# Performance work log

Measured on AMD Instinct MI355X. Metric: run time of the kernel, lower is better.

## Reference

```python
import jax, jax.numpy as jnp
import numpy as np

DIM = 1024
N_HEADS = 16
HEAD_DIM = DIM // N_HEADS


def setup_inputs() -> dict:
    key = jax.random.key(0)
    ks = jax.random.split(key, 7)
    s = 1.0 / np.sqrt(DIM)
    return {
        "hidden_states": jax.random.normal(ks[0], (1, 4096, DIM), dtype=jnp.float32),
        "Wq": jax.random.uniform(ks[1], (DIM, DIM), jnp.float32, -s, s),
        "bq": jax.random.uniform(ks[2], (DIM,), jnp.float32, -s, s),
        "Wk": jax.random.uniform(ks[3], (DIM, DIM), jnp.float32, -s, s),
        "bk": jax.random.uniform(ks[4], (DIM,), jnp.float32, -s, s),
        "Wv": jax.random.uniform(ks[5], (DIM, DIM), jnp.float32, -s, s),
        "bv": jax.random.uniform(ks[6], (DIM,), jnp.float32, -s, s),
    }


def _split_heads(x):
    # [B, S, DIM] -> [B, H, S, HEAD_DIM]
    b, s, _ = x.shape
    return x.reshape(b, s, N_HEADS, HEAD_DIM).transpose(0, 2, 1, 3)


def reference(hidden_states, Wq, bq, Wk, bk, Wv, bv):
    q = _split_heads(hidden_states @ Wq + bq)
    k = _split_heads(hidden_states @ Wk + bk)
    v = _split_heads(hidden_states @ Wv + bv)
    scores = jnp.einsum("bhqd,bhkd->bhqk", q, k) / np.sqrt(HEAD_DIM).astype(np.float32)
    probs = jax.nn.softmax(scores, axis=-1)  # dropout prob = 0 -> identity
    ctx = jnp.einsum("bhqk,bhkd->bhqd", probs, v)
    b, h, s, d = ctx.shape
    return ctx.transpose(0, 2, 1, 3).reshape(b, s, h * d)
```

## Files before the change

kernel.cpp:

```cpp
#include <hip/hip_runtime.h>
#include <hip/hip_bf16.h>

#define S_LEN 4096
#define DIM   1024
#define NH    16
#define HD    64

typedef unsigned short u16;
typedef short  bf16x8 __attribute__((ext_vector_type(8)));
typedef float  f32x4  __attribute__((ext_vector_type(4)));

__device__ __forceinline__ u16 f2bf(float f){
  union { float f; unsigned u; } x; x.f = f;
  unsigned u = x.u;
  return (u16)((u + 0x7FFFu + ((u >> 16) & 1u)) >> 16);
}
__device__ __forceinline__ unsigned pk2(float a, float b){
  union { __hip_bfloat162 h; unsigned u; } x;
  x.h = __float22bfloat162_rn(float2{a, b});
  return x.u;
}
__device__ __forceinline__ void ld2lds16(const u16* g, u16* l){
  __builtin_amdgcn_global_load_lds((const __attribute__((address_space(1))) void*)g,
                                   (__attribute__((address_space(3))) void*)l, 16, 0, 0);
}

#define QSCALE 0.1803368801111204f

__global__ __launch_bounds__(256) void fill_sentinel(float* __restrict__ out, int n){
  int i = blockIdx.x * 256 + threadIdx.x;
  if (i < n) out[i] = 77.0f;
}

__global__ __launch_bounds__(256) void prep_fused(
    const float* __restrict__ X, u16* __restrict__ Xb,
    const float* __restrict__ W0, const float* __restrict__ W1, const float* __restrict__ W2,
    u16* __restrict__ Wt)
{
  __shared__ __align__(16) u16 tile[64*72];
  int b = blockIdx.x;
  int t = threadIdx.x;
  if (b < 2048){
    size_t i = ((size_t)b * 256 + t) * 8;
    float4 v0 = *(const float4*)(X + i);
    float4 v1 = *(const float4*)(X + i + 4);
    uint4 w;
    w.x = pk2(v0.x, v0.y); w.y = pk2(v0.z, v0.w);
    w.z = pk2(v1.x, v1.y); w.w = pk2(v1.z, v1.w);
    *(uint4*)(Xb + i) = w;
    return;
  }
  int tid = b - 2048;
  int z   = tid >> 8;
  int rem = tid & 255;
  int k0  = (rem & 15) * 64, n0 = (rem >> 4) * 64;
  const float* W = z==0 ? W0 : z==1 ? W1 : W2;
  u16* T = Wt + (size_t)z * DIM * DIM;
  #pragma unroll
  for (int i = 0; i < 4; ++i){
    int idx = t + i*256;
    int row = idx >> 4, col4 = (idx & 15) * 4;
    float4 v = *(const float4*)(W + (size_t)(k0+row)*DIM + n0 + col4);
    tile[(col4+0)*72 + row] = f2bf(v.x);
    tile[(col4+1)*72 + row] = f2bf(v.y);
    tile[(col4+2)*72 + row] = f2bf(v.z);
    tile[(col4+3)*72 + row] = f2bf(v.w);
  }
  __syncthreads();
  #pragma unroll
  for (int i = 0; i < 2; ++i){
    int idx = t + i*256;
    int n = idx >> 3, k16 = (idx & 7) * 8;
    *(int4*)(T + (size_t)(n0+n)*DIM + k0 + k16) = *(const int4*)(tile + n*72 + k16);
  }
}

__device__ __forceinline__ void qkv_epilogue(
    int z, int m0, int n0, int wm, int wn, int quad, int l15,
    const f32x4 acc[4][4], const float* bias,
    u16* __restrict__ qb, u16* __restrict__ kf_out, u16* __restrict__ vf_out)
{
  #pragma unroll
  for (int nt=0; nt<4; ++nt){
    int n = n0 + wn + nt*16 + l15;
    float bv = bias[n];
    int h = n >> 6, d = n & 63;
    #pragma unroll
    for (int mt=0; mt<4; ++mt){
      int mb = m0 + wm + mt*16 + quad*4;
      f32x4 c = acc[mt][nt];
      if (z == 0){
        #pragma unroll
        for (int r=0; r<4; ++r)
          qb[(size_t)(mb + r)*DIM + n] = f2bf((c[r] + bv) * QSCALE);
      } else if (z == 1){
        int half = d >> 5, quadk = (d >> 3) & 3, j = d & 7;
        #pragma unroll
        for (int r=0; r<4; ++r){
          int s = mb + r;
          size_t idx = ((((size_t)h*256 + (s >> 4))*2 + half)*64 + quadk*16 + (s & 15))*8 + j;
          kf_out[idx] = f2bf(c[r] + bv);
        }
      } else {
        int kt64 = mb >> 6;
        int kn   = (mb >> 4) & 3;
        int qsl  = (mb >> 2) & 3;
        int h2   = kn >> 1;
        int jj0  = (kn & 1) * 4;
        int dt = d >> 4, dl = d & 15;
        size_t base = (((((size_t)h*64 + kt64)*4 + dt)*2 + h2)*64 + qsl*16 + dl)*8 + jj0;
        ushort4 p;
        p.x = f2bf(c[0]+bv); p.y = f2bf(c[1]+bv);
        p.z = f2bf(c[2]+bv); p.w = f2bf(c[3]+bv);
        *(ushort4*)(vf_out + base) = p;
      }
    }
  }
}

__global__ __launch_bounds__(256) void qkv_gemm_fast(
    const u16* __restrict__ Xbf, const u16* __restrict__ Wt,
    const float* __restrict__ b0, const float* __restrict__ b1, const float* __restrict__ b2,
    u16* __restrict__ qb, u16* __restrict__ kf_out, u16* __restrict__ vf_out)
{
  int fid = blockIdx.x;
  int z   = fid >> 8;
  int r   = fid & 255;
  int m0  = (((r & 7) << 2) + ((r >> 3) & 3)) * 128;
  int n0  = (r >> 5) * 128;

  const u16* Wz = Wt + (size_t)z * DIM * DIM;
  const float* bias = z==0 ? b0 : z==1 ? b1 : b2;

  __shared__ __align__(16) u16 SMEM[128*136];
  u16* As = SMEM;
  u16* Bs = SMEM + 8192;

  int t = threadIdx.x, wave = t >> 6, lane = t & 63, quad = lane >> 4, l15 = lane & 15;
  int wm = (wave >> 1) * 64, wn = (wave & 1) * 64;

  f32x4 acc[4][4];
  #pragma unroll
  for (int i=0;i<4;++i)
    #pragma unroll
    for (int j=0;j<4;++j) acc[i][j] = (f32x4){0.f,0.f,0.f,0.f};

  int srow = wave*32 + (lane >> 2);
  int skc_g = (((lane & 3) ^ ((lane >> 3) & 3))) * 8;
  int skc_l = (lane & 3) * 8;
  const u16* gA0 = Xbf + (size_t)(m0 + srow)*DIM + skc_g;
  const u16* gA1 = gA0 + (size_t)16*DIM;
  const u16* gB0 = Wz  + (size_t)(n0 + srow)*DIM + skc_g;
  const u16* gB1 = gB0 + (size_t)16*DIM;
  u16* lA0 = As + srow*32 + skc_l;
  u16* lA1 = lA0 + 16*32;
  u16* lB0 = Bs + srow*32 + skc_l;
  u16* lB1 = lB0 + 16*32;

  int swz = (quad ^ ((l15 >> 1) & 3)) * 8;

#define GSTAGE(P, KO)                                                            \
  do {                                                                           \
    ld2lds16(gA0 + (KO), lA0 + (P)*4096);                                        \
    ld2lds16(gA1 + (KO), lA1 + (P)*4096);                                        \
    ld2lds16(gB0 + (KO), lB0 + (P)*4096);                                        \
    ld2lds16(gB1 + (KO), lB1 + (P)*4096);                                        \
  } while(0)

#define GCOMPUTE(P)                                                              \
  do {                                                                           \
    bf16x8 af[4], bfr[4];                                                        \
    _Pragma("unroll")                                                            \
    for (int mt=0; mt<4; ++mt) af[mt]  = *(const bf16x8*)(As + (P)*4096 + (wm + mt*16 + l15)*32 + swz); \
    _Pragma("unroll")                                                            \
    for (int nt=0; nt<4; ++nt) bfr[nt] = *(const bf16x8*)(Bs + (P)*4096 + (wn + nt*16 + l15)*32 + swz); \
    _Pragma("unroll")                                                            \
    for (int mt=0; mt<4; ++mt)                                                   \
      _Pragma("unroll")                                                          \
      for (int nt=0; nt<4; ++nt)                                                 \
        acc[mt][nt] = __builtin_amdgcn_mfma_f32_16x16x32_bf16(af[mt], bfr[nt], acc[mt][nt], 0, 0, 0); \
  } while(0)

  GSTAGE(0, 0);
  __syncthreads();

  for (int kt = 0; kt < 32; kt += 2){
    GSTAGE(1, (kt+1)*32);
    GCOMPUTE(0);
    __syncthreads();
    if (kt + 2 < 32) GSTAGE(0, (kt+2)*32);
    GCOMPUTE(1);
    __syncthreads();
  }

#undef GSTAGE
#undef GCOMPUTE

  #pragma unroll
  for (int nt=0; nt<4; ++nt){
    int nl = wn + nt*16 + l15;
    int n  = n0 + nl;
    float bv = bias[n];
    #pragma unroll
    for (int mt=0; mt<4; ++mt){
      int mbl = wm + mt*16 + quad*4;
      f32x4 c = acc[mt][nt];
      if (z == 0){
        #pragma unroll
        for (int rr=0; rr<4; ++rr)
          SMEM[(mbl+rr)*136 + nl] = f2bf((c[rr] + bv) * QSCALE);
      } else if (z == 1){
        #pragma unroll
        for (int rr=0; rr<4; ++rr)
          SMEM[(mbl+rr)*136 + nl] = f2bf(c[rr] + bv);
      } else {
        int k64l = (mbl >> 6) & 1;
        int kn   = (mbl >> 4) & 3;
        int qsl  = (mbl >> 2) & 3;
        int h2   = kn >> 1;
        int jj0  = (kn & 1) * 4;
        int hh   = wn >> 6;
        int dt   = nt;
        int addr = ((((hh*2 + k64l)*4 + dt)*2 + h2)*64 + qsl*16 + l15)*8 + jj0;
        ushort4 p;
        p.x = f2bf(c[0]+bv); p.y = f2bf(c[1]+bv);
        p.z = f2bf(c[2]+bv); p.w = f2bf(c[3]+bv);
        *(ushort4*)(SMEM + addr) = p;
      }
    }
  }
  __syncthreads();

  if (z == 0){
    #pragma unroll
    for (int i=0; i<8; ++i){
      int u = t + i*256;
      int row = u >> 4, cu = u & 15;
      *(uint4*)(qb + (size_t)(m0+row)*DIM + n0 + cu*8) =
          *(const uint4*)(SMEM + row*136 + cu*8);
    }
  } else if (z == 1){
    #pragma unroll
    for (int i=0; i<8; ++i){
      int u = t + i*256;
      int c  = u >> 6;
      int w  = u & 63;
      int qk = w >> 4, sk = w & 15;
      int g  = c >> 2, hh = (c >> 1) & 1, half = c & 1;
      int hgl = (n0 >> 6) + hh;
      size_t dst = ((((size_t)hgl*256 + (m0>>4) + g)*2 + half)*64 + qk*16 + sk)*8;
      *(uint4*)(kf_out + dst) =
          *(const uint4*)(SMEM + (g*16+sk)*136 + hh*64 + half*32 + qk*8);
    }
  } else {
    #pragma unroll
    for (int i=0; i<8; ++i){
      int u = t + i*256;
      int chunk = u >> 9;
      int w = u & 511;
      int hh = chunk >> 1, k64l = chunk & 1;
      int hgl = (n0 >> 6) + hh;
      size_t dst = ((size_t)hgl*64 + (m0>>6) + k64l)*4096 + (size_t)w*8;
      *(uint4*)(vf_out + dst) = *(const uint4*)(SMEM + chunk*4096 + w*8);
    }
  }
}

__global__ __launch_bounds__(256) void qkv_gemm_legacy(
    const float* __restrict__ X,
    const float* __restrict__ Wq, const float* __restrict__ Wk, const float* __restrict__ Wv,
    const float* __restrict__ b0, const float* __restrict__ b1, const float* __restrict__ b2,
    u16* __restrict__ qb, u16* __restrict__ kf_out, u16* __restrict__ vf_out)
{
  int z = blockIdx.z;
  const float* W    = z==0 ? Wq : z==1 ? Wk : Wv;
  const float* bias = z==0 ? b0 : z==1 ? b1 : b2;

  __shared__ __align__(16) u16 As[128*40];
  __shared__ __align__(16) u16 Bs[128*40];

  int m0 = blockIdx.x * 128, n0 = blockIdx.y * 128;
  int t = threadIdx.x, wave = t >> 6, lane = t & 63, quad = lane >> 4, l15 = lane & 15;
  int wm = (wave >> 1) * 64, wn = (wave & 1) * 64;

  f32x4 acc[4][4];
  #pragma unroll
  for (int i=0;i<4;++i)
    #pragma unroll
    for (int j=0;j<4;++j) acc[i][j] = (f32x4){0.f,0.f,0.f,0.f};

  int sr = t >> 2, sc = (t & 3) * 8;
  const float* gA0 = X + (size_t)(m0 + sr) * DIM + sc;
  const float* gA1 = X + (size_t)(m0 + 64 + sr) * DIM + sc;
  int br = t >> 3, bc = (t & 7) * 16;
  const float* gW = W + (size_t)br * DIM + n0 + bc;

  for (int kt = 0; kt < 32; ++kt){
    int ko = kt * 32;
    float4 a00 = *(const float4*)(gA0 + ko);
    float4 a01 = *(const float4*)(gA0 + ko + 4);
    float4 a10 = *(const float4*)(gA1 + ko);
    float4 a11 = *(const float4*)(gA1 + ko + 4);
    float4 w0  = *(const float4*)(gW + (size_t)ko*DIM);
    float4 w1  = *(const float4*)(gW + (size_t)ko*DIM + 4);
    float4 w2  = *(const float4*)(gW + (size_t)ko*DIM + 8);
    float4 w3  = *(const float4*)(gW + (size_t)ko*DIM + 12);
    int4 pa0, pa1;
    pa0.x = pk2(a00.x,a00.y); pa0.y = pk2(a00.z,a00.w);
    pa0.z = pk2(a01.x,a01.y); pa0.w = pk2(a01.z,a01.w);
    pa1.x = pk2(a10.x,a10.y); pa1.y = pk2(a10.z,a10.w);
    pa1.z = pk2(a11.x,a11.y); pa1.w = pk2(a11.z,a11.w);
    u16 wb[16];
    wb[0]=f2bf(w0.x); wb[1]=f2bf(w0.y); wb[2]=f2bf(w0.z); wb[3]=f2bf(w0.w);
    wb[4]=f2bf(w1.x); wb[5]=f2bf(w1.y); wb[6]=f2bf(w1.z); wb[7]=f2bf(w1.w);
    wb[8]=f2bf(w2.x); wb[9]=f2bf(w2.y); wb[10]=f2bf(w2.z); wb[11]=f2bf(w2.w);
    wb[12]=f2bf(w3.x); wb[13]=f2bf(w3.y); wb[14]=f2bf(w3.z); wb[15]=f2bf(w3.w);
    __syncthreads();
    *(int4*)(As + sr*40 + sc)      = pa0;
    *(int4*)(As + (64+sr)*40 + sc) = pa1;
    #pragma unroll
    for (int j=0;j<16;++j) Bs[(bc+j)*40 + br] = wb[j];
    __syncthreads();
    bf16x8 af[4], bfr[4];
    #pragma unroll
    for (int mt=0; mt<4; ++mt) af[mt]  = *(const bf16x8*)(As + (wm + mt*16 + l15)*40 + quad*8);
    #pragma unroll
    for (int nt=0; nt<4; ++nt) bfr[nt] = *(const bf16x8*)(Bs + (wn + nt*16 + l15)*40 + quad*8);
    #pragma unroll
    for (int mt=0; mt<4; ++mt)
      #pragma unroll
      for (int nt=0; nt<4; ++nt)
        acc[mt][nt] = __builtin_amdgcn_mfma_f32_16x16x32_bf16(af[mt], bfr[nt], acc[mt][nt], 0, 0, 0);
  }
  qkv_epilogue(z, m0, n0, wm, wn, quad, l15, acc, bias, qb, kf_out, vf_out);
}

__global__ __launch_bounds__(256, 2) void attn(
    const u16* __restrict__ Qb, const u16* __restrict__ Kf,
    const u16* __restrict__ Vf, float* __restrict__ out)
{
  int fid = blockIdx.x;
  int xcd  = fid & 7;
  int hpar = (fid >> 3) & 1;
  int qb   = fid >> 4;
  int h    = xcd*2 + hpar;

  int t = threadIdx.x, wave = t >> 6, lane = t & 63, quad = lane >> 4, l15 = lane & 15;
  int q0 = qb * 128 + wave * 32;
  int dg = (wave ^ (fid >> 8)) & 1;

  __shared__ __align__(16) u16 Ks0[4096], Ks1[4096], Vs0[4096], Vs1[4096];

  const u16* Kfh = Kf + (size_t)h * 262144;
  const u16* Vfh = Vf + (size_t)h * 262144;

  bf16x8 qf[2][2];
  #pragma unroll
  for (int qs=0; qs<2; ++qs){
    const u16* Qp = Qb + (size_t)(q0 + qs*16 + l15)*DIM + h*HD;
    qf[qs][0] = *(const bf16x8*)(Qp + quad*8);
    qf[qs][1] = *(const bf16x8*)(Qp + 32 + quad*8);
  }

  f32x4 O[2][4];
  #pragma unroll
  for (int qs=0; qs<2; ++qs)
    #pragma unroll
    for (int dt=0; dt<4; ++dt) O[qs][dt] = (f32x4){0.f,0.f,0.f,0.f};
  float lsum[2] = {0.f, 0.f};

  typedef union { uint4 u; bf16x8 v; } pfu;

#define STAGE(KS, VS, T)                                                         \
  do {                                                                           \
    const u16* kg_ = Kfh + (size_t)(T)*4096 + t*8;                               \
    ld2lds16(kg_,        KS + t*8);                                              \
    ld2lds16(kg_ + 2048, KS + t*8 + 2048);                                       \
    const u16* vg_ = Vfh + (size_t)(T)*4096 + t*8;                               \
    ld2lds16(vg_,        VS + t*8);                                              \
    ld2lds16(vg_ + 2048, VS + t*8 + 2048);                                       \
  } while(0)

#define QK_EXP(KS, PF)                                                           \
  do {                                                                           \
    bf16x8 kfr[4][2];                                                            \
    _Pragma("unroll")                                                            \
    for (int kn=0; kn<4; ++kn)                                                   \
      _Pragma("unroll")                                                          \
      for (int hf=0; hf<2; ++hf)                                                 \
        kfr[kn][hf] = *(const bf16x8*)((KS) + (kn*2+hf)*512 + lane*8);           \
    f32x4 st[2][4];                                                              \
    __builtin_amdgcn_s_setprio(1);                                               \
    _Pragma("unroll")                                                            \
    for (int qs=0; qs<2; ++qs)                                                   \
      _Pragma("unroll")                                                          \
      for (int kn=0; kn<4; ++kn){                                                \
        f32x4 zz = (f32x4){0.f,0.f,0.f,0.f};                                     \
        zz = __builtin_amdgcn_mfma_f32_16x16x32_bf16(kfr[kn][0], qf[qs][0], zz, 0,0,0); \
        zz = __builtin_amdgcn_mfma_f32_16x16x32_bf16(kfr[kn][1], qf[qs][1], zz, 0,0,0); \
        st[qs][kn] = zz;                                                         \
      }                                                                          \
    __builtin_amdgcn_s_setprio(0);                                               \
    _Pragma("unroll")                                                            \
    for (int qs=0; qs<2; ++qs){                                                  \
      float ls = 0.f;                                                            \
      _Pragma("unroll")                                                          \
      for (int kn=0; kn<4; ++kn)                                                 \
        _Pragma("unroll")                                                        \
        for (int r=0; r<4; ++r){                                                 \
          float p = __builtin_amdgcn_exp2f(st[qs][kn][r]);                       \
          st[qs][kn][r] = p; ls += p;                                            \
        }                                                                        \
      lsum[qs] += ls;                                                            \
      PF[qs][0].u.x = pk2(st[qs][0][0], st[qs][0][1]);                           \
      PF[qs][0].u.y = pk2(st[qs][0][2], st[qs][0][3]);                           \
      PF[qs][0].u.z = pk2(st[qs][1][0], st[qs][1][1]);                           \
      PF[qs][0].u.w = pk2(st[qs][1][2], st[qs][1][3]);                           \
      PF[qs][1].u.x = pk2(st[qs][2][0], st[qs][2][1]);                           \
      PF[qs][1].u.y = pk2(st[qs][2][2], st[qs][2][3]);                           \
      PF[qs][1].u.z = pk2(st[qs][3][0], st[qs][3][1]);                           \
      PF[qs][1].u.w = pk2(st[qs][3][2], st[qs][3][3]);                           \
    }                                                                            \
  } while(0)

#define LOADV(VFR, VS)                                                           \
  do {                                                                           \
    _Pragma("unroll")                                                            \
    for (int dt=0; dt<4; ++dt)                                                   \
      _Pragma("unroll")                                                          \
      for (int c2=0; c2<2; ++c2)                                                 \
        VFR[dt][c2] = *(const bf16x8*)((VS) + (dt*2+c2)*512 + lane*8);           \
  } while(0)

#define PV(PF, VFR)                                                              \
  do {                                                                           \
    __builtin_amdgcn_s_setprio(1);                                               \
    _Pragma("unroll")                                                            \
    for (int qs=0; qs<2; ++qs)                                                   \
      _Pragma("unroll")                                                          \
      for (int dt=0; dt<4; ++dt){                                                \
        f32x4 o = O[qs][dt];                                                     \
        o = __builtin_amdgcn_mfma_f32_16x16x32_bf16(VFR[dt][0], PF[qs][0].v, o, 0,0,0); \
        o = __builtin_amdgcn_mfma_f32_16x16x32_bf16(VFR[dt][1], PF[qs][1].v, o, 0,0,0); \
        O[qs][dt] = o;                                                           \
      }                                                                          \
    __builtin_amdgcn_s_setprio(0);                                               \
  } while(0)

#define COMPUTE(KS, VS, FIRST)                                                   \
  do {                                                                           \
    if (!dg){                                                                    \
      pfu pfN[2][2]; bf16x8 vfrN[4][2];                                          \
      QK_EXP(KS, pfN);                                                           \
      LOADV(vfrN, VS);                                                           \
      PV(pfN, vfrN);                                                             \
    } else {                                                                     \
      if (!(FIRST)) PV(pfC, vfrC);                                               \
      QK_EXP(KS, pfC);                                                           \
      LOADV(vfrC, VS);                                                           \
    }                                                                            \
  } while(0)

  pfu pfC[2][2];
  bf16x8 vfrC[4][2];

  STAGE(Ks0, Vs0, 0);
  __syncthreads();
  STAGE(Ks1, Vs1, 1);
  COMPUTE(Ks0, Vs0, 1);
  __syncthreads();

  for (int kt = 1; kt < 63; kt += 2){
    STAGE(Ks0, Vs0, kt+1);
    COMPUTE(Ks1, Vs1, 0);
    __syncthreads();
    STAGE(Ks1, Vs1, kt+2);
    COMPUTE(Ks0, Vs0, 0);
    __syncthreads();
  }
  COMPUTE(Ks1, Vs1, 0);
  if (dg) PV(pfC, vfrC);

#undef STAGE
#undef QK_EXP
#undef LOADV
#undef PV
#undef COMPUTE

  #pragma unroll
  for (int qs=0; qs<2; ++qs){
    float l = lsum[qs];
    l += __shfl_xor(l, 16, 64);
    l += __shfl_xor(l, 32, 64);
    float inv = 1.0f / l;
    int query = q0 + qs*16 + l15;
    #pragma unroll
    for (int dt=0; dt<4; ++dt){
      float4 v;
      v.x = O[qs][dt][0]*inv; v.y = O[qs][dt][1]*inv;
      v.z = O[qs][dt][2]*inv; v.w = O[qs][dt][3]*inv;
      *(float4*)(out + (size_t)query*DIM + h*HD + dt*16 + quad*4) = v;
    }
  }
}

extern "C" void kernel_launch(void* const* d_in, const int* in_sizes, int n_in,
                              void* d_out, int out_size, void* d_ws, size_t ws_size,
                              hipStream_t stream)
{
  const float* X  = (const float*)d_in[0];
  const float* Wq = (const float*)d_in[1];
  const float* bq = (const float*)d_in[2];
  const float* Wk = (const float*)d_in[3];
  const float* bk = (const float*)d_in[4];
  const float* Wv = (const float*)d_in[5];
  const float* bv = (const float*)d_in[6];
  float* out = (float*)d_out;
  u16*   ws  = (u16*)d_ws;

  const size_t SD = (size_t)S_LEN * DIM;
  const size_t need_fast = (4*SD + 3*(size_t)DIM*DIM) * sizeof(u16);
  const size_t need_min  = (size_t)24 * 1024 * 1024;

  if (ws_size >= need_fast){
    u16* xbf = ws;
    u16* wt  = xbf + SD;
    u16* qb  = wt + 3*(size_t)DIM*DIM;
    u16* kf  = qb + SD;
    u16* vf  = kf + SD;
    prep_fused   <<<dim3(2048 + 768), 256, 0, stream>>>(X, xbf, Wq, Wk, Wv, wt);
    qkv_gemm_fast<<<dim3(768), 256, 0, stream>>>(xbf, wt, bq, bk, bv, qb, kf, vf);
    attn         <<<dim3(512), 256, 0, stream>>>(qb, kf, vf, out);
  } else if (ws_size >= need_min){
    u16* qb = ws;
    u16* kf = qb + SD;
    u16* vf = kf + SD;
    qkv_gemm_legacy<<<dim3(32, 8, 3), 256, 0, stream>>>(X, Wq, Wk, Wv, bq, bk, bv, qb, kf, vf);
    attn           <<<dim3(512), 256, 0, stream>>>(qb, kf, vf, out);
  } else {
    fill_sentinel<<<(out_size + 255)/256, 256, 0, stream>>>(out, out_size);
  }
}
```

Measured before the change: 193.8 us.

## Split attention over two KV halves with a separate combine kernel

Adds a split-KV attention path. Each of 1024 blocks processes half of the key/value sequence and writes unnormalized fp32 partial outputs and row sums to workspace. A second kernel adds the two halves and normalizes. This doubles the grid to raise occupancy and parallelism on the 256-CU device (launch bounds 4), at the cost of 32MB of extra partial-output traffic and an additional kernel launch. The path runs only when the workspace is large enough, otherwise the old single-pass kernel is used.

Measured after the change: 453.7 us. 2.34x slower.

```diff
diff --git a/kernel.cpp b/kernel.cpp
--- a/kernel.cpp
+++ b/kernel.cpp
@@ -335,43 +335,9 @@
   qkv_epilogue(z, m0, n0, wm, wn, quad, l15, acc, bias, qb, kf_out, vf_out);
 }
 
-__global__ __launch_bounds__(256, 2) void attn(
-    const u16* __restrict__ Qb, const u16* __restrict__ Kf,
-    const u16* __restrict__ Vf, float* __restrict__ out)
-{
-  int fid = blockIdx.x;
-  int xcd  = fid & 7;
-  int hpar = (fid >> 3) & 1;
-  int qb   = fid >> 4;
-  int h    = xcd*2 + hpar;
-
-  int t = threadIdx.x, wave = t >> 6, lane = t & 63, quad = lane >> 4, l15 = lane & 15;
-  int q0 = qb * 128 + wave * 32;
-  int dg = (wave ^ (fid >> 8)) & 1;
-
-  __shared__ __align__(16) u16 Ks0[4096], Ks1[4096], Vs0[4096], Vs1[4096];
-
-  const u16* Kfh = Kf + (size_t)h * 262144;
-  const u16* Vfh = Vf + (size_t)h * 262144;
-
-  bf16x8 qf[2][2];
-  #pragma unroll
-  for (int qs=0; qs<2; ++qs){
-    const u16* Qp = Qb + (size_t)(q0 + qs*16 + l15)*DIM + h*HD;
-    qf[qs][0] = *(const bf16x8*)(Qp + quad*8);
-    qf[qs][1] = *(const bf16x8*)(Qp + 32 + quad*8);
-  }
-
-  f32x4 O[2][4];
-  #pragma unroll
-  for (int qs=0; qs<2; ++qs)
-    #pragma unroll
-    for (int dt=0; dt<4; ++dt) O[qs][dt] = (f32x4){0.f,0.f,0.f,0.f};
-  float lsum[2] = {0.f, 0.f};
-
-  typedef union { uint4 u; bf16x8 v; } pfu;
-
-#define STAGE(KS, VS, T)                                                         \
+typedef union { uint4 u; bf16x8 v; } pfu;
+
+#define ATT_STAGE(KS, VS, T)                                                     \
   do {                                                                           \
     const u16* kg_ = Kfh + (size_t)(T)*4096 + t*8;                               \
     ld2lds16(kg_,        KS + t*8);                                              \
@@ -381,7 +347,7 @@
     ld2lds16(vg_ + 2048, VS + t*8 + 2048);                                       \
   } while(0)
 
-#define QK_EXP(KS, PF)                                                           \
+#define ATT_QK_EXP(KS, PF)                                                       \
   do {                                                                           \
     bf16x8 kfr[4][2];                                                            \
     _Pragma("unroll")                                                            \
@@ -423,7 +389,7 @@
     }                                                                            \
   } while(0)
 
-#define LOADV(VFR, VS)                                                           \
+#define ATT_LOADV(VFR, VS)                                                       \
   do {                                                                           \
     _Pragma("unroll")                                                            \
     for (int dt=0; dt<4; ++dt)                                                   \
@@ -432,7 +398,7 @@
         VFR[dt][c2] = *(const bf16x8*)((VS) + (dt*2+c2)*512 + lane*8);           \
   } while(0)
 
-#define PV(PF, VFR)                                                              \
+#define ATT_PV(PF, VFR)                                                          \
   do {                                                                           \
     __builtin_amdgcn_s_setprio(1);                                               \
     _Pragma("unroll")                                                            \
@@ -447,45 +413,73 @@
     __builtin_amdgcn_s_setprio(0);                                               \
   } while(0)
 
-#define COMPUTE(KS, VS, FIRST)                                                   \
+#define ATT_COMPUTE(KS, VS, FIRST)                                               \
   do {                                                                           \
     if (!dg){                                                                    \
       pfu pfN[2][2]; bf16x8 vfrN[4][2];                                          \
-      QK_EXP(KS, pfN);                                                           \
-      LOADV(vfrN, VS);                                                           \
-      PV(pfN, vfrN);                                                             \
+      ATT_QK_EXP(KS, pfN);                                                       \
+      ATT_LOADV(vfrN, VS);                                                       \
+      ATT_PV(pfN, vfrN);                                                         \
     } else {                                                                     \
-      if (!(FIRST)) PV(pfC, vfrC);                                               \
-      QK_EXP(KS, pfC);                                                           \
-      LOADV(vfrC, VS);                                                           \
+      if (!(FIRST)) ATT_PV(pfC, vfrC);                                           \
+      ATT_QK_EXP(KS, pfC);                                                       \
+      ATT_LOADV(vfrC, VS);                                                       \
     }                                                                            \
   } while(0)
 
+__global__ __launch_bounds__(256, 2) void attn(
+    const u16* __restrict__ Qb, const u16* __restrict__ Kf,
+    const u16* __restrict__ Vf, float* __restrict__ out)
+{
+  int fid = blockIdx.x;
+  int xcd  = fid & 7;
+  int hpar = (fid >> 3) & 1;
+  int qb   = fid >> 4;
+  int h    = xcd*2 + hpar;
+
+  int t = threadIdx.x, wave = t >> 6, lane = t & 63, quad = lane >> 4, l15 = lane & 15;
+  int q0 = qb * 128 + wave * 32;
+  int dg = (wave ^ (fid >> 8)) & 1;
+
+  __shared__ __align__(16) u16 Ks0[4096], Ks1[4096], Vs0[4096], Vs1[4096];
+
+  const u16* Kfh = Kf + (size_t)h * 262144;
+  const u16* Vfh = Vf + (size_t)h * 262144;
+
+  bf16x8 qf[2][2];
+  #pragma unroll
+  for (int qs=0; qs<2; ++qs){
+    const u16* Qp = Qb + (size_t)(q0 + qs*16 + l15)*DIM + h*HD;
+    qf[qs][0] = *(const bf16x8*)(Qp + quad*8);
+    qf[qs][1] = *(const bf16x8*)(Qp + 32 + quad*8);
+  }
+
+  f32x4 O[2][4];
+  #pragma unroll
+  for (int qs=0; qs<2; ++qs)
+    #pragma unroll
+    for (int dt=0; dt<4; ++dt) O[qs][dt] = (f32x4){0.f,0.f,0.f,0.f};
+  float lsum[2] = {0.f, 0.f};
+
   pfu pfC[2][2];
   bf16x8 vfrC[4][2];
 
-  STAGE(Ks0, Vs0, 0);
+  ATT_STAGE(Ks0, Vs0, 0);
   __syncthreads();
-  STAGE(Ks1, Vs1, 1);
-  COMPUTE(Ks0, Vs0, 1);
+  ATT_STAGE(Ks1, Vs1, 1);
+  ATT_COMPUTE(Ks0, Vs0, 1);
   __syncthreads();
 
   for (int kt = 1; kt < 63; kt += 2){
-    STAGE(Ks0, Vs0, kt+1);
-    COMPUTE(Ks1, Vs1, 0);
-    __syncthreads();
-    STAGE(Ks1, Vs1, kt+2);
-    COMPUTE(Ks0, Vs0, 0);
-    __syncthreads();
-  }
-  COMPUTE(Ks1, Vs1, 0);
-  if (dg) PV(pfC, vfrC);
-
-#undef STAGE
-#undef QK_EXP
-#undef LOADV
-#undef PV
-#undef COMPUTE
+    ATT_STAGE(Ks0, Vs0, kt+1);
+    ATT_COMPUTE(Ks1, Vs1, 0);
+    __syncthreads();
+    ATT_STAGE(Ks1, Vs1, kt+2);
+    ATT_COMPUTE(Ks0, Vs0, 0);
+    __syncthreads();
+  }
+  ATT_COMPUTE(Ks1, Vs1, 0);
+  if (dg) ATT_PV(pfC, vfrC);
 
   #pragma unroll
   for (int qs=0; qs<2; ++qs){
@@ -502,6 +496,101 @@
       *(float4*)(out + (size_t)query*DIM + h*HD + dt*16 + quad*4) = v;
     }
   }
+}
+
+__global__ __launch_bounds__(256, 4) void attn_split(
+    const u16* __restrict__ Qb, const u16* __restrict__ Kf,
+    const u16* __restrict__ Vf, float* __restrict__ op, float* __restrict__ lp)
+{
+  int fid = blockIdx.x;
+  int xcd  = fid & 7;
+  int hpar = (fid >> 3) & 1;
+  int qb   = (fid >> 4) & 31;
+  int half = (fid >> 9) & 1;
+  int h    = xcd*2 + hpar;
+  int base = half * 32;
+
+  int t = threadIdx.x, wave = t >> 6, lane = t & 63, quad = lane >> 4, l15 = lane & 15;
+  int q0 = qb * 128 + wave * 32;
+  int dg = (wave ^ (fid >> 8)) & 1;
+
+  __shared__ __align__(16) u16 Ks0[4096], Ks1[4096], Vs0[4096], Vs1[4096];
+
+  const u16* Kfh = Kf + (size_t)h * 262144;
+  const u16* Vfh = Vf + (size_t)h * 262144;
+
+  float* opH = op + (size_t)half * (S_LEN*DIM);
+  float* lpH = lp + (size_t)half * (NH*S_LEN);
+
+  bf16x8 qf[2][2];
+  #pragma unroll
+  for (int qs=0; qs<2; ++qs){
+    const u16* Qp = Qb + (size_t)(q0 + qs*16 + l15)*DIM + h*HD;
+    qf[qs][0] = *(const bf16x8*)(Qp + quad*8);
+    qf[qs][1] = *(const bf16x8*)(Qp + 32 + quad*8);
+  }
+
+  f32x4 O[2][4];
+  #pragma unroll
+  for (int qs=0; qs<2; ++qs)
+    #pragma unroll
+    for (int dt=0; dt<4; ++dt) O[qs][dt] = (f32x4){0.f,0.f,0.f,0.f};
+  float lsum[2] = {0.f, 0.f};
+
+  pfu pfC[2][2];
+  bf16x8 vfrC[4][2];
+
+  ATT_STAGE(Ks0, Vs0, base);
+  __syncthreads();
+  ATT_STAGE(Ks1, Vs1, base+1);
+  ATT_COMPUTE(Ks0, Vs0, 1);
+  __syncthreads();
+
+  for (int kt = 1; kt < 31; kt += 2){
+    ATT_STAGE(Ks0, Vs0, base+kt+1);
+    ATT_COMPUTE(Ks1, Vs1, 0);
+    __syncthreads();
+    ATT_STAGE(Ks1, Vs1, base+kt+2);
+    ATT_COMPUTE(Ks0, Vs0, 0);
+    __syncthreads();
+  }
+  ATT_COMPUTE(Ks1, Vs1, 0);
+  if (dg) ATT_PV(pfC, vfrC);
+
+  #pragma unroll
+  for (int qs=0; qs<2; ++qs){
+    float l = lsum[qs];
+    l += __shfl_xor(l, 16, 64);
+    l += __shfl_xor(l, 32, 64);
+    int query = q0 + qs*16 + l15;
+    if (quad == 0) lpH[h*S_LEN + query] = l;
+    #pragma unroll
+    for (int dt=0; dt<4; ++dt){
+      float4 v;
+      v.x = O[qs][dt][0]; v.y = O[qs][dt][1];
+      v.z = O[qs][dt][2]; v.w = O[qs][dt][3];
+      *(float4*)(opH + (size_t)query*DIM + h*HD + dt*16 + quad*4) = v;
+    }
+  }
+}
+
+__global__ __launch_bounds__(256) void attn_combine(
+    const float* __restrict__ op, const float* __restrict__ lp, float* __restrict__ out)
+{
+  size_t idx = ((size_t)blockIdx.x * 256 + threadIdx.x) * 4;
+  int q = (int)(idx >> 10);
+  int c = (int)(idx & 1023);
+  int h = c >> 6;
+  float l = lp[h*S_LEN + q] + lp[NH*S_LEN + h*S_LEN + q];
+  float inv = 1.0f / l;
+  float4 a = *(const float4*)(op + idx);
+  float4 b = *(const float4*)(op + (size_t)S_LEN*DIM + idx);
+  float4 r;
+  r.x = (a.x + b.x) * inv;
+  r.y = (a.y + b.y) * inv;
+  r.z = (a.z + b.z) * inv;
+  r.w = (a.w + b.w) * inv;
+  *(float4*)(out + idx) = r;
 }
 
 extern "C" void kernel_launch(void* const* d_in, const int* in_sizes, int n_in,
@@ -519,8 +608,9 @@
   u16*   ws  = (u16*)d_ws;
 
   const size_t SD = (size_t)S_LEN * DIM;
-  const size_t need_fast = (4*SD + 3*(size_t)DIM*DIM) * sizeof(u16);
-  const size_t need_min  = (size_t)24 * 1024 * 1024;
+  const size_t need_fast  = (4*SD + 3*(size_t)DIM*DIM) * sizeof(u16);
+  const size_t need_split = need_fast + (2*SD + 2*(size_t)NH*S_LEN) * sizeof(float);
+  const size_t need_min   = (size_t)24 * 1024 * 1024;
 
   if (ws_size >= need_fast){
     u16* xbf = ws;
@@ -530,7 +620,14 @@
     u16* vf  = kf + SD;
     prep_fused   <<<dim3(2048 + 768), 256, 0, stream>>>(X, xbf, Wq, Wk, Wv, wt);
     qkv_gemm_fast<<<dim3(768), 256, 0, stream>>>(xbf, wt, bq, bk, bv, qb, kf, vf);
-    attn         <<<dim3(512), 256, 0, stream>>>(qb, kf, vf, out);
+    if (ws_size >= need_split){
+      float* op = (float*)(vf + SD);
+      float* lp = op + 2*SD;
+      attn_split  <<<dim3(1024), 256, 0, stream>>>(qb, kf, vf, op, lp);
+      attn_combine<<<dim3((int)(SD/4/256)), 256, 0, stream>>>(op, lp, out);
+    } else {
+      attn        <<<dim3(512), 256, 0, stream>>>(qb, kf, vf, out);
+    }
   } else if (ws_size >= need_min){
     u16* qb = ws;
     u16* kf = qb + SD;
```
